# Optimization experiments

Measured on AMD Instinct MI355X. Metric: run time of the kernel, lower is better.

The kernel has to match this reference:

```python
import jax, jax.numpy as jnp
import numpy as np


def _conv1x1(x, w, b):
    # x: (B,C,H,W), w: (O,C), b: (O,)
    return jnp.einsum('bchw,oc->bohw', x, w) + b[None, :, None, None]


def setup_inputs() -> dict:
    key = jax.random.key(0)
    ks = jax.random.split(key, 10)
    B, C, H, W = 8, 64, 64, 64
    x = jax.random.normal(ks[0], (B, C, H, W), dtype=jnp.float32)
    s = 0.05
    params = {}
    names = ['wq', 'wQ', 'wK', 'wV']
    for i, n in enumerate(names):
        params[n] = jax.random.normal(ks[1 + 2 * i], (C, C), dtype=jnp.float32) * s
        params['b' + n[1:]] = jax.random.normal(ks[2 + 2 * i], (C,), dtype=jnp.float32) * s
    return dict(x=x, wq=params['wq'], bq=params['bq'], wQ=params['wQ'], bQ=params['bQ'],
                wK=params['wK'], bK=params['bK'], wV=params['wV'], bV=params['bV'],
                gamma=jnp.ones((1,), dtype=jnp.float32))


def reference(x, wq, bq, wQ, bQ, wK, bK, wV, bV, gamma):
    B, C, H, W = x.shape
    # q = query_conv(x).view(B,-1,W,H)  (pure reshape, matches torch .view on contiguous tensor)
    q = _conv1x1(x, wq, bq).reshape(B, C, W, H)
    # 2x2 average pool, stride 2
    qp = q.reshape(B, C, W // 2, 2, H // 2, 2).mean(axis=(3, 5))
    q_ = qp.reshape(B, C, (W * H) // 4)          # (B, C, N/4)
    K = _conv1x1(x, wK, bK).reshape(B, C, H * W)  # (B, C, N)
    V = _conv1x1(x, wV, bV).reshape(B, C, H * W)  # (B, C, N)
    # stage 1: pooled queries attend over all keys
    attn1 = jax.nn.softmax(jnp.einsum('bcp,bcn->bpn', q_, K), axis=-1)  # (B, N/4, N)
    out = jnp.einsum('bcn,bpn->bcp', V, attn1)                           # (B, C, N/4)
    # stage 2: full queries attend over pooled anchors
    Q = _conv1x1(x, wQ, bQ).reshape(B, C, H * W)                         # (B, C, N)
    attn2 = jax.nn.softmax(jnp.einsum('bcn,bcp->bnp', Q, q_), axis=-1)   # (B, N, N/4)
    out = jnp.einsum('bcp,bnp->bcn', out, attn2)                         # (B, C, N)
    out = out.reshape(B, C, H, W)
    return gamma * out + x
```

## Files before the change

### kernel.cpp

```cpp
#include <hip/hip_runtime.h>
#include <hip/hip_bf16.h>


typedef float  f32x4  __attribute__((ext_vector_type(4)));
typedef __bf16 bf16x8 __attribute__((ext_vector_type(8)));
typedef __bf16 bf16x4 __attribute__((ext_vector_type(4)));

__device__ __forceinline__ int swz(int ch) { return ch ^ ((ch >> 3) & 7); }

__global__ __launch_bounds__(256) void conv4_kernel(
    const float* __restrict__ x,
    const float* __restrict__ wq, const float* __restrict__ bq,
    const float* __restrict__ wQ, const float* __restrict__ bQ,
    const float* __restrict__ wK, const float* __restrict__ bK,
    const float* __restrict__ wV, const float* __restrict__ bV,
    __bf16* __restrict__ Kt, __bf16* __restrict__ Vc,
    __bf16* __restrict__ Qt, __bf16* __restrict__ qt)
{
  __shared__ float xs[64 * 132];
  __shared__ float wsh[64 * 68];

  const int tid = threadIdx.x;
  const int m   = blockIdx.x >> 8;
  const int b   = (blockIdx.x >> 5) & 7;
  const int rp  = blockIdx.x & 31;
  const int n0  = rp << 7;

  const float* wg = (m == 0) ? wK : (m == 1) ? wV : (m == 2) ? wQ : wq;
  const float* bg = (m == 0) ? bK : (m == 1) ? bV : (m == 2) ? bQ : bq;

  for (int i = tid; i < 64 * 32; i += 256) {
    int c = i >> 5, j = i & 31;
    *(f32x4*)&xs[c * 132 + j * 4] =
        *(const f32x4*)&x[((size_t)(b * 64 + c)) * 4096 + n0 + j * 4];
  }
  for (int i = tid; i < 1024; i += 256) {
    int o = i >> 4, c0 = (i & 15) << 2;
    f32x4 v = *(const f32x4*)&wg[o * 64 + c0];
    wsh[(c0 + 0) * 68 + o] = v[0];
    wsh[(c0 + 1) * 68 + o] = v[1];
    wsh[(c0 + 2) * 68 + o] = v[2];
    wsh[(c0 + 3) * 68 + o] = v[3];
  }
  __syncthreads();

  const int ty = tid >> 4, tx = tid & 15;

  float acc[4][8];
  {
    f32x4 bv = *(const f32x4*)&bg[ty * 4];
#pragma unroll
    for (int i = 0; i < 4; ++i)
#pragma unroll
      for (int j = 0; j < 8; ++j) acc[i][j] = bv[i];
  }

#pragma unroll 4
  for (int c = 0; c < 64; ++c) {
    f32x4 wv = *(const f32x4*)&wsh[c * 68 + ty * 4];
    f32x4 xa = *(const f32x4*)&xs[c * 132 + tx * 8];
    f32x4 xb = *(const f32x4*)&xs[c * 132 + tx * 8 + 4];
#pragma unroll
    for (int i = 0; i < 4; ++i) {
#pragma unroll
      for (int j = 0; j < 4; ++j) {
        acc[i][j]     += wv[i] * xa[j];
        acc[i][j + 4] += wv[i] * xb[j];
      }
    }
  }

  if (m == 0 || m == 2) {
    __bf16* dst = (m == 0) ? Kt : Qt;
#pragma unroll
    for (int j = 0; j < 8; ++j) {
      int n = n0 + tx * 8 + j;
      bf16x4 pk;
#pragma unroll
      for (int i = 0; i < 4; ++i) pk[i] = (__bf16)acc[i][j];
      *(bf16x4*)&dst[((size_t)(b * 4096 + n)) * 64 + ty * 4] = pk;
    }
  } else if (m == 1) {
#pragma unroll
    for (int i = 0; i < 4; ++i) {
      int o = ty * 4 + i;
      bf16x8 pk;
#pragma unroll
      for (int j = 0; j < 8; ++j) pk[j] = (__bf16)acc[i][j];
      *(bf16x8*)&Vc[((size_t)(b * 64 + o)) * 4096 + n0 + tx * 8] = pk;
    }
  } else {
    float pl[4][4];
#pragma unroll
    for (int i = 0; i < 4; ++i)
#pragma unroll
      for (int jj = 0; jj < 4; ++jj)
        pl[i][jj] = acc[i][2 * jj] + acc[i][2 * jj + 1];
#pragma unroll
    for (int i = 0; i < 4; ++i)
#pragma unroll
      for (int jj = 0; jj < 4; ++jj)
        pl[i][jj] += __shfl_xor(pl[i][jj], 8);
    if (tx < 8) {
#pragma unroll
      for (int jj = 0; jj < 4; ++jj) {
        int p = rp * 32 + tx * 4 + jj;
        bf16x4 pk;
#pragma unroll
        for (int i = 0; i < 4; ++i) pk[i] = (__bf16)(0.25f * pl[i][jj]);
        *(bf16x4*)&qt[((size_t)(b * 1024 + p)) * 64 + ty * 4] = pk;
      }
    }
  }
}

__global__ __launch_bounds__(512, 2) void attn1_kernel(
    const __bf16* __restrict__ Qg,
    const __bf16* __restrict__ Kg,
    const __bf16* __restrict__ Vg,
    __bf16* __restrict__ partOb,
    float* __restrict__ partL)
{
  __shared__ __align__(16) char smem[65536];

  const int tid = threadIdx.x;
  const int w = tid >> 6, lane = tid & 63;
  const int lg = (lane >> 4) & 3, lp = lane & 15;
  const int b   = blockIdx.x >> 6;
  const int qb  = (blockIdx.x >> 4) & 3;
  const int ks  = blockIdx.x & 15;

  bf16x8 qf[2][2];
#pragma unroll
  for (int qs = 0; qs < 2; ++qs) {
    const __bf16* qg =
        Qg + ((size_t)(b * 1024 + qb * 256 + w * 32 + qs * 16 + lp)) * 64;
    qf[qs][0] = *(const bf16x8*)(qg + lg * 8);
    qf[qs][1] = *(const bf16x8*)(qg + 32 + lg * 8);
  }

  f32x4 acc[2][4];
#pragma unroll
  for (int qs = 0; qs < 2; ++qs)
#pragma unroll
    for (int ct = 0; ct < 4; ++ct) acc[qs][ct] = (f32x4){0.f, 0.f, 0.f, 0.f};
  float l_run[2] = {0.f, 0.f};

  bf16x8 kreg, vreg;
  const int swt = swz(tid);
  auto load_tile = [&](int r) {
    const int kv0 = ks * 256 + r * 64;
    kreg = *(const bf16x8*)(Kg + ((size_t)(b * 4096 + kv0 + (tid >> 3))) * 64 +
                            (tid & 7) * 8);
    vreg = *(const bf16x8*)(Vg + ((size_t)(b * 64 + (tid >> 3))) * 4096 + kv0 +
                            (tid & 7) * 8);
  };
  auto write_tile = [&](int nb) {
    *(bf16x8*)((__bf16*)(smem + nb * 8192) + swt * 8) = kreg;
    *(bf16x8*)((__bf16*)(smem + 16384 + nb * 8192) + swt * 8) = vreg;
  };

  load_tile(0); write_tile(0); load_tile(1);
  __syncthreads();

  for (int r = 0; r < 4; ++r) {
    const int cur = r & 1;
    if (r + 1 < 4) write_tile(cur ^ 1);
    if (r + 2 < 4) load_tile(r + 2);

    const __bf16* lK = (const __bf16*)(smem + cur * 8192);
    const __bf16* lV = (const __bf16*)(smem + 16384 + cur * 8192);
    __bf16* lP = (__bf16*)(smem + 32768) + w * 2048;

    bf16x8 ka[4][2];
#pragma unroll
    for (int mt = 0; mt < 4; ++mt) {
      int ch0 = (mt * 16 + lp) * 8 + lg;
      ka[mt][0] = *(const bf16x8*)(lK + swz(ch0) * 8);
      ka[mt][1] = *(const bf16x8*)(lK + swz(ch0 + 4) * 8);
    }

#pragma unroll
    for (int qs = 0; qs < 2; ++qs) {
      f32x4 S[4];
#pragma unroll
      for (int mt = 0; mt < 4; ++mt) {
        f32x4 z = (f32x4){0.f, 0.f, 0.f, 0.f};
        z = __builtin_amdgcn_mfma_f32_16x16x32_bf16(ka[mt][0], qf[qs][0], z, 0, 0, 0);
        z = __builtin_amdgcn_mfma_f32_16x16x32_bf16(ka[mt][1], qf[qs][1], z, 0, 0, 0);
        S[mt] = z;
      }

      float rs = 0.f;
#pragma unroll
      for (int mt = 0; mt < 4; ++mt)
#pragma unroll
        for (int rr = 0; rr < 4; ++rr) {
          float e = __expf(S[mt][rr]);
          S[mt][rr] = e;
          rs += e;
        }
      rs += __shfl_xor(rs, 16);
      rs += __shfl_xor(rs, 32);
      l_run[qs] += rs;

#pragma unroll
      for (int mt = 0; mt < 4; ++mt) {
        bf16x4 pk;
#pragma unroll
        for (int rr = 0; rr < 4; ++rr) pk[rr] = (__bf16)S[mt][rr];
        int boff = (qs * 16 + lp) * 128 + mt * 32 + lg * 8;
        *(bf16x4*)((char*)lP + (boff ^ ((lp & 7) << 4))) = pk;
      }
    }

    bf16x8 pf[2][2];
#pragma unroll
    for (int qs = 0; qs < 2; ++qs) {
      int chp = (qs * 16 + lp) * 8 + lg;
      pf[qs][0] = *(const bf16x8*)(lP + swz(chp) * 8);
      pf[qs][1] = *(const bf16x8*)(lP + swz(chp + 4) * 8);
    }
#pragma unroll
    for (int ct = 0; ct < 4; ++ct) {
      int chv = (ct * 16 + lp) * 8 + lg;
      bf16x8 v0 = *(const bf16x8*)(lV + swz(chv) * 8);
      bf16x8 v1 = *(const bf16x8*)(lV + swz(chv + 4) * 8);
#pragma unroll
      for (int qs = 0; qs < 2; ++qs) {
        acc[qs][ct] = __builtin_amdgcn_mfma_f32_16x16x32_bf16(v0, pf[qs][0], acc[qs][ct], 0, 0, 0);
        acc[qs][ct] = __builtin_amdgcn_mfma_f32_16x16x32_bf16(v1, pf[qs][1], acc[qs][ct], 0, 0, 0);
      }
    }
    __syncthreads();
  }

  const int gq = w * 32;
  const size_t pbase = (size_t)((b * 4 + qb) * 16 + ks);
  if (lg == 0) {
#pragma unroll
    for (int qs = 0; qs < 2; ++qs)
      partL[pbase * 256 + gq + qs * 16 + lp] = l_run[qs];
  }
  __bf16* po = partOb + pbase * 16384;
#pragma unroll
  for (int qs = 0; qs < 2; ++qs)
#pragma unroll
    for (int ct = 0; ct < 4; ++ct)
#pragma unroll
      for (int rr = 0; rr < 4; ++rr)
        po[(ct * 16 + lg * 4 + rr) * 256 + gq + qs * 16 + lp] =
            (__bf16)acc[qs][ct][rr];
}

__global__ __launch_bounds__(256) void combine1_kernel(
    const __bf16* __restrict__ partOb, const float* __restrict__ partL,
    __bf16* __restrict__ O1)
{
  __shared__ float linv[256];

  const int tid = threadIdx.x;
  const int b   = blockIdx.x >> 5;
  const int qb  = (blockIdx.x >> 3) & 3;
  const int cs  = blockIdx.x & 7;
  const size_t rbase = (size_t)((b * 4 + qb) * 16);

  {
    float l = 0.f;
#pragma unroll
    for (int s = 0; s < 16; ++s) l += partL[(rbase + s) * 256 + tid];
    linv[tid] = 1.0f / l;
  }
  __syncthreads();

  const int c = cs * 8 + (tid >> 5), q8 = (tid & 31) * 8;
  float o[8] = {0.f, 0.f, 0.f, 0.f, 0.f, 0.f, 0.f, 0.f};
#pragma unroll
  for (int s = 0; s < 16; ++s) {
    bf16x8 v = *(const bf16x8*)(partOb + (rbase + s) * 16384 + c * 256 + q8);
#pragma unroll
    for (int j = 0; j < 8; ++j) o[j] += (float)v[j];
  }
  bf16x8 pk;
#pragma unroll
  for (int j = 0; j < 8; ++j) pk[j] = (__bf16)(o[j] * linv[q8 + j]);
  *(bf16x8*)(O1 + ((size_t)(b * 64 + c)) * 1024 + qb * 256 + q8) = pk;
}

__global__ __launch_bounds__(512, 2) void attn2_kernel(
    const __bf16* __restrict__ Qg,
    const __bf16* __restrict__ Kg,
    const __bf16* __restrict__ Vg,
    float* __restrict__ outp,
    const float* __restrict__ xres,
    const float* __restrict__ gammap)
{
  __shared__ __align__(16) char smem[98304];

  const int tid = threadIdx.x;
  const int w = tid >> 6, lane = tid & 63;
  const int lg = (lane >> 4) & 3, lp = lane & 15;
  const int qg4 = w & 3, ks = w >> 2;
  const int b  = blockIdx.x >> 5;
  const int q0 = (blockIdx.x & 31) * 128;

  bf16x8 qf[2][2];
#pragma unroll
  for (int qs = 0; qs < 2; ++qs) {
    const __bf16* qg =
        Qg + ((size_t)(b * 4096 + q0 + qg4 * 32 + qs * 16 + lp)) * 64;
    qf[qs][0] = *(const bf16x8*)(qg + lg * 8);
    qf[qs][1] = *(const bf16x8*)(qg + 32 + lg * 8);
  }

  f32x4 acc[2][4];
#pragma unroll
  for (int qs = 0; qs < 2; ++qs)
#pragma unroll
    for (int ct = 0; ct < 4; ++ct) acc[qs][ct] = (f32x4){0.f, 0.f, 0.f, 0.f};
  float l_run[2] = {0.f, 0.f};

  bf16x8 kreg[2], vreg[2];
  const int csi = tid & 255, sp = tid >> 8;
  const int sw0 = swz(csi), sw1 = swz(csi + 256);
  auto load_tile = [&](int r) {
    const int a0 = sp * 512 + r * 64;
#pragma unroll
    for (int j = 0; j < 2; ++j) {
      int s = csi + j * 256;
      int row = s >> 3, col = (s & 7) * 8;
      kreg[j] = *(const bf16x8*)(Kg + ((size_t)(b * 1024 + a0 + row)) * 64 + col);
      vreg[j] = *(const bf16x8*)(Vg + ((size_t)(b * 64 + row)) * 1024 + a0 + col);
    }
  };
  auto write_tile = [&](int nb) {
    __bf16* kd = (__bf16*)(smem + (sp * 2 + nb) * 8192);
    __bf16* vd = (__bf16*)(smem + 32768 + (sp * 2 + nb) * 8192);
    *(bf16x8*)(kd + sw0 * 8) = kreg[0];
    *(bf16x8*)(kd + sw1 * 8) = kreg[1];
    *(bf16x8*)(vd + sw0 * 8) = vreg[0];
    *(bf16x8*)(vd + sw1 * 8) = vreg[1];
  };

  load_tile(0); write_tile(0); load_tile(1);
  __syncthreads();

  for (int r = 0; r < 8; ++r) {
    const int cur = r & 1;
    if (r + 1 < 8) write_tile(cur ^ 1);
    if (r + 2 < 8) load_tile(r + 2);

    const __bf16* lK = (const __bf16*)(smem + (ks * 2 + cur) * 8192);
    const __bf16* lV = (const __bf16*)(smem + 32768 + (ks * 2 + cur) * 8192);
    __bf16* lP = (__bf16*)(smem + 65536) + w * 2048;

    bf16x8 ka[4][2];
#pragma unroll
    for (int mt = 0; mt < 4; ++mt) {
      int ch0 = (mt * 16 + lp) * 8 + lg;
      ka[mt][0] = *(const bf16x8*)(lK + swz(ch0) * 8);
      ka[mt][1] = *(const bf16x8*)(lK + swz(ch0 + 4) * 8);
    }

#pragma unroll
    for (int qs = 0; qs < 2; ++qs) {
      f32x4 S[4];
#pragma unroll
      for (int mt = 0; mt < 4; ++mt) {
        f32x4 z = (f32x4){0.f, 0.f, 0.f, 0.f};
        z = __builtin_amdgcn_mfma_f32_16x16x32_bf16(ka[mt][0], qf[qs][0], z, 0, 0, 0);
        z = __builtin_amdgcn_mfma_f32_16x16x32_bf16(ka[mt][1], qf[qs][1], z, 0, 0, 0);
        S[mt] = z;
      }

      float rs = 0.f;
#pragma unroll
      for (int mt = 0; mt < 4; ++mt)
#pragma unroll
        for (int rr = 0; rr < 4; ++rr) {
          float e = __expf(S[mt][rr]);
          S[mt][rr] = e;
          rs += e;
        }
      rs += __shfl_xor(rs, 16);
      rs += __shfl_xor(rs, 32);
      l_run[qs] += rs;

#pragma unroll
      for (int mt = 0; mt < 4; ++mt) {
        bf16x4 pk;
#pragma unroll
        for (int rr = 0; rr < 4; ++rr) pk[rr] = (__bf16)S[mt][rr];
        int boff = (qs * 16 + lp) * 128 + mt * 32 + lg * 8;
        *(bf16x4*)((char*)lP + (boff ^ ((lp & 7) << 4))) = pk;
      }
    }

    bf16x8 pf[2][2];
#pragma unroll
    for (int qs = 0; qs < 2; ++qs) {
      int chp = (qs * 16 + lp) * 8 + lg;
      pf[qs][0] = *(const bf16x8*)(lP + swz(chp) * 8);
      pf[qs][1] = *(const bf16x8*)(lP + swz(chp + 4) * 8);
    }
#pragma unroll
    for (int ct = 0; ct < 4; ++ct) {
      int chv = (ct * 16 + lp) * 8 + lg;
      bf16x8 v0 = *(const bf16x8*)(lV + swz(chv) * 8);
      bf16x8 v1 = *(const bf16x8*)(lV + swz(chv + 4) * 8);
#pragma unroll
      for (int qs = 0; qs < 2; ++qs) {
        acc[qs][ct] = __builtin_amdgcn_mfma_f32_16x16x32_bf16(v0, pf[qs][0], acc[qs][ct], 0, 0, 0);
        acc[qs][ct] = __builtin_amdgcn_mfma_f32_16x16x32_bf16(v1, pf[qs][1], acc[qs][ct], 0, 0, 0);
      }
    }
    __syncthreads();
  }

  float* cb = (float*)smem;
  float* lb = (float*)(smem + 69632);
  if (lg == 0) {
#pragma unroll
    for (int qs = 0; qs < 2; ++qs)
      lb[w * 32 + qs * 16 + lp] = l_run[qs];
  }
  {
    float* myc = cb + w * 2176;
#pragma unroll
    for (int qs = 0; qs < 2; ++qs)
#pragma unroll
      for (int ct = 0; ct < 4; ++ct)
        *(f32x4*)(myc + (qs * 16 + lp) * 68 + ct * 16 + lg * 4) = acc[qs][ct];
  }
  __syncthreads();

  if (w < 4) {
    const int g = w;
    const float g0 = gammap[0];
#pragma unroll
    for (int qs = 0; qs < 2; ++qs) {
      const int qq = qs * 16 + lp;
      const int nq = q0 + g * 32 + qq;
      float inv = 1.0f / (lb[g * 32 + qq] + lb[(g + 4) * 32 + qq]);
#pragma unroll
      for (int ct = 0; ct < 4; ++ct) {
        f32x4 t0 = *(const f32x4*)(cb + g * 2176 + qq * 68 + ct * 16 + lg * 4);
        f32x4 t1 = *(const f32x4*)(cb + (g + 4) * 2176 + qq * 68 + ct * 16 + lg * 4);
        f32x4 o = t0 + t1;
#pragma unroll
        for (int rr = 0; rr < 4; ++rr) {
          int c = ct * 16 + lg * 4 + rr;
          size_t oi = ((size_t)(b * 64 + c)) * 4096 + nq;
          outp[oi] = g0 * (o[rr] * inv) + xres[oi];
        }
      }
    }
  }
}

extern "C" void kernel_launch(void* const* d_in, const int* in_sizes, int n_in,
                              void* d_out, int out_size, void* d_ws, size_t ws_size,
                              hipStream_t stream) {
  const float* x     = (const float*)d_in[0];
  const float* wq    = (const float*)d_in[1];
  const float* bq    = (const float*)d_in[2];
  const float* wQ    = (const float*)d_in[3];
  const float* bQ    = (const float*)d_in[4];
  const float* wK    = (const float*)d_in[5];
  const float* bK    = (const float*)d_in[6];
  const float* wV    = (const float*)d_in[7];
  const float* bV    = (const float*)d_in[8];
  const float* gamma = (const float*)d_in[9];

  __bf16* ws = (__bf16*)d_ws;
  __bf16* Kt = ws;
  __bf16* Vc = ws + 2097152;
  __bf16* Qt = ws + 4194304;
  __bf16* qt = ws + 6291456;
  __bf16* O1 = ws + 6815744;
  __bf16* partOb1 = (__bf16*)((char*)d_ws + (16ull << 20));
  float*  partL1  = (float*)((char*)d_ws + (33ull << 20));

  hipLaunchKernelGGL(conv4_kernel, dim3(1024), dim3(256), 0, stream,
                     x, wq, bq, wQ, bQ, wK, bK, wV, bV, Kt, Vc, Qt, qt);
  hipLaunchKernelGGL(attn1_kernel, dim3(512), dim3(512), 0, stream,
                     qt, Kt, Vc, partOb1, partL1);
  hipLaunchKernelGGL(combine1_kernel, dim3(256), dim3(256), 0, stream,
                     partOb1, partL1, O1);
  hipLaunchKernelGGL(attn2_kernel, dim3(256), dim3(512), 0, stream,
                     Qt, qt, O1, (float*)d_out, x, gamma);
}
```

Baseline: 66.52 us.

## Read V fragments directly from global memory and transpose PV MFMA output layout

In both attention kernels, V tiles are no longer staged through shared memory. Each wave loads its V MFMA fragments straight from global memory, relying on V's channel-major layout, and swaps the MFMA operand order so the accumulator comes out transposed. That layout lets the partial-output stores and the final residual epilogue use vectorized bf16x4/f32x4 accesses, and it shrinks LDS usage. The cost is redundant global/L2 reads of V across waves, issued on the critical path without prefetching.

```diff
diff --git a/kernel.cpp b/kernel.cpp
--- a/kernel.cpp
+++ b/kernel.cpp
@@ -121,7 +121,7 @@
     __bf16* __restrict__ partOb,
     float* __restrict__ partL)
 {
-  __shared__ __align__(16) char smem[65536];
+  __shared__ __align__(16) char smem[49152];
 
   const int tid = threadIdx.x;
   const int w = tid >> 6, lane = tid & 63;
@@ -146,18 +146,15 @@
     for (int ct = 0; ct < 4; ++ct) acc[qs][ct] = (f32x4){0.f, 0.f, 0.f, 0.f};
   float l_run[2] = {0.f, 0.f};
 
-  bf16x8 kreg, vreg;
+  bf16x8 kreg;
   const int swt = swz(tid);
   auto load_tile = [&](int r) {
     const int kv0 = ks * 256 + r * 64;
     kreg = *(const bf16x8*)(Kg + ((size_t)(b * 4096 + kv0 + (tid >> 3))) * 64 +
                             (tid & 7) * 8);
-    vreg = *(const bf16x8*)(Vg + ((size_t)(b * 64 + (tid >> 3))) * 4096 + kv0 +
-                            (tid & 7) * 8);
   };
   auto write_tile = [&](int nb) {
     *(bf16x8*)((__bf16*)(smem + nb * 8192) + swt * 8) = kreg;
-    *(bf16x8*)((__bf16*)(smem + 16384 + nb * 8192) + swt * 8) = vreg;
   };
 
   load_tile(0); write_tile(0); load_tile(1);
@@ -168,9 +165,9 @@
     if (r + 1 < 4) write_tile(cur ^ 1);
     if (r + 2 < 4) load_tile(r + 2);
 
+    const int kv0 = ks * 256 + r * 64;
     const __bf16* lK = (const __bf16*)(smem + cur * 8192);
-    const __bf16* lV = (const __bf16*)(smem + 16384 + cur * 8192);
-    __bf16* lP = (__bf16*)(smem + 32768) + w * 2048;
+    __bf16* lP = (__bf16*)(smem + 16384) + w * 2048;
 
     bf16x8 ka[4][2];
 #pragma unroll
@@ -223,13 +220,13 @@
     }
 #pragma unroll
     for (int ct = 0; ct < 4; ++ct) {
-      int chv = (ct * 16 + lp) * 8 + lg;
-      bf16x8 v0 = *(const bf16x8*)(lV + swz(chv) * 8);
-      bf16x8 v1 = *(const bf16x8*)(lV + swz(chv + 4) * 8);
+      const __bf16* vr = Vg + ((size_t)(b * 64 + ct * 16 + lp)) * 4096 + kv0 + lg * 8;
+      bf16x8 vf0 = *(const bf16x8*)(vr);
+      bf16x8 vf1 = *(const bf16x8*)(vr + 32);
 #pragma unroll
       for (int qs = 0; qs < 2; ++qs) {
-        acc[qs][ct] = __builtin_amdgcn_mfma_f32_16x16x32_bf16(v0, pf[qs][0], acc[qs][ct], 0, 0, 0);
-        acc[qs][ct] = __builtin_amdgcn_mfma_f32_16x16x32_bf16(v1, pf[qs][1], acc[qs][ct], 0, 0, 0);
+        acc[qs][ct] = __builtin_amdgcn_mfma_f32_16x16x32_bf16(pf[qs][0], vf0, acc[qs][ct], 0, 0, 0);
+        acc[qs][ct] = __builtin_amdgcn_mfma_f32_16x16x32_bf16(pf[qs][1], vf1, acc[qs][ct], 0, 0, 0);
       }
     }
     __syncthreads();
@@ -246,11 +243,12 @@
 #pragma unroll
   for (int qs = 0; qs < 2; ++qs)
 #pragma unroll
-    for (int ct = 0; ct < 4; ++ct)
-#pragma unroll
-      for (int rr = 0; rr < 4; ++rr)
-        po[(ct * 16 + lg * 4 + rr) * 256 + gq + qs * 16 + lp] =
-            (__bf16)acc[qs][ct][rr];
+    for (int ct = 0; ct < 4; ++ct) {
+      bf16x4 pk;
+#pragma unroll
+      for (int rr = 0; rr < 4; ++rr) pk[rr] = (__bf16)acc[qs][ct][rr];
+      *(bf16x4*)&po[(ct * 16 + lp) * 256 + gq + qs * 16 + lg * 4] = pk;
+    }
 }
 
 __global__ __launch_bounds__(256) void combine1_kernel(
@@ -295,7 +293,7 @@
     const float* __restrict__ xres,
     const float* __restrict__ gammap)
 {
-  __shared__ __align__(16) char smem[98304];
+  __shared__ __align__(16) char smem[74752];
 
   const int tid = threadIdx.x;
   const int w = tid >> 6, lane = tid & 63;
@@ -320,7 +318,7 @@
     for (int ct = 0; ct < 4; ++ct) acc[qs][ct] = (f32x4){0.f, 0.f, 0.f, 0.f};
   float l_run[2] = {0.f, 0.f};
 
-  bf16x8 kreg[2], vreg[2];
+  bf16x8 kreg[2];
   const int csi = tid & 255, sp = tid >> 8;
   const int sw0 = swz(csi), sw1 = swz(csi + 256);
   auto load_tile = [&](int r) {
@@ -330,16 +328,12 @@
       int s = csi + j * 256;
       int row = s >> 3, col = (s & 7) * 8;
       kreg[j] = *(const bf16x8*)(Kg + ((size_t)(b * 1024 + a0 + row)) * 64 + col);
-      vreg[j] = *(const bf16x8*)(Vg + ((size_t)(b * 64 + row)) * 1024 + a0 + col);
     }
   };
   auto write_tile = [&](int nb) {
     __bf16* kd = (__bf16*)(smem + (sp * 2 + nb) * 8192);
-    __bf16* vd = (__bf16*)(smem + 32768 + (sp * 2 + nb) * 8192);
     *(bf16x8*)(kd + sw0 * 8) = kreg[0];
     *(bf16x8*)(kd + sw1 * 8) = kreg[1];
-    *(bf16x8*)(vd + sw0 * 8) = vreg[0];
-    *(bf16x8*)(vd + sw1 * 8) = vreg[1];
   };
 
   load_tile(0); write_tile(0); load_tile(1);
@@ -350,9 +344,9 @@
     if (r + 1 < 8) write_tile(cur ^ 1);
     if (r + 2 < 8) load_tile(r + 2);
 
+    const int kv0 = ks * 512 + r * 64;
     const __bf16* lK = (const __bf16*)(smem + (ks * 2 + cur) * 8192);
-    const __bf16* lV = (const __bf16*)(smem + 32768 + (ks * 2 + cur) * 8192);
-    __bf16* lP = (__bf16*)(smem + 65536) + w * 2048;
+    __bf16* lP = (__bf16*)(smem + 32768) + w * 2048;
 
     bf16x8 ka[4][2];
 #pragma unroll
@@ -405,32 +399,32 @@
     }
 #pragma unroll
     for (int ct = 0; ct < 4; ++ct) {
-      int chv = (ct * 16 + lp) * 8 + lg;
-      bf16x8 v0 = *(const bf16x8*)(lV + swz(chv) * 8);
-      bf16x8 v1 = *(const bf16x8*)(lV + swz(chv + 4) * 8);
+      const __bf16* vr = Vg + ((size_t)(b * 64 + ct * 16 + lp)) * 1024 + kv0 + lg * 8;
+      bf16x8 vf0 = *(const bf16x8*)(vr);
+      bf16x8 vf1 = *(const bf16x8*)(vr + 32);
 #pragma unroll
       for (int qs = 0; qs < 2; ++qs) {
-        acc[qs][ct] = __builtin_amdgcn_mfma_f32_16x16x32_bf16(v0, pf[qs][0], acc[qs][ct], 0, 0, 0);
-        acc[qs][ct] = __builtin_amdgcn_mfma_f32_16x16x32_bf16(v1, pf[qs][1], acc[qs][ct], 0, 0, 0);
+        acc[qs][ct] = __builtin_amdgcn_mfma_f32_16x16x32_bf16(pf[qs][0], vf0, acc[qs][ct], 0, 0, 0);
+        acc[qs][ct] = __builtin_amdgcn_mfma_f32_16x16x32_bf16(pf[qs][1], vf1, acc[qs][ct], 0, 0, 0);
       }
     }
     __syncthreads();
   }
 
   float* cb = (float*)smem;
-  float* lb = (float*)(smem + 69632);
+  float* lb = (float*)(smem + 73728);
   if (lg == 0) {
 #pragma unroll
     for (int qs = 0; qs < 2; ++qs)
       lb[w * 32 + qs * 16 + lp] = l_run[qs];
   }
   {
-    float* myc = cb + w * 2176;
+    float* myc = cb + w * 2304;
 #pragma unroll
     for (int qs = 0; qs < 2; ++qs)
 #pragma unroll
       for (int ct = 0; ct < 4; ++ct)
-        *(f32x4*)(myc + (qs * 16 + lp) * 68 + ct * 16 + lg * 4) = acc[qs][ct];
+        *(f32x4*)(myc + (ct * 16 + lp) * 36 + qs * 16 + lg * 4) = acc[qs][ct];
   }
   __syncthreads();
 
@@ -439,20 +433,24 @@
     const float g0 = gammap[0];
 #pragma unroll
     for (int qs = 0; qs < 2; ++qs) {
-      const int qq = qs * 16 + lp;
-      const int nq = q0 + g * 32 + qq;
-      float inv = 1.0f / (lb[g * 32 + qq] + lb[(g + 4) * 32 + qq]);
+      f32x4 lv0 = *(const f32x4*)(lb + g * 32 + qs * 16 + lg * 4);
+      f32x4 lv1 = *(const f32x4*)(lb + (g + 4) * 32 + qs * 16 + lg * 4);
+      f32x4 inv4;
+#pragma unroll
+      for (int j = 0; j < 4; ++j) inv4[j] = 1.0f / (lv0[j] + lv1[j]);
 #pragma unroll
       for (int ct = 0; ct < 4; ++ct) {
-        f32x4 t0 = *(const f32x4*)(cb + g * 2176 + qq * 68 + ct * 16 + lg * 4);
-        f32x4 t1 = *(const f32x4*)(cb + (g + 4) * 2176 + qq * 68 + ct * 16 + lg * 4);
-        f32x4 o = t0 + t1;
-#pragma unroll
-        for (int rr = 0; rr < 4; ++rr) {
-          int c = ct * 16 + lg * 4 + rr;
-          size_t oi = ((size_t)(b * 64 + c)) * 4096 + nq;
-          outp[oi] = g0 * (o[rr] * inv) + xres[oi];
-        }
+        int coff = (ct * 16 + lp) * 36 + qs * 16 + lg * 4;
+        f32x4 t0 = *(const f32x4*)(cb + g * 2304 + coff);
+        f32x4 t1 = *(const f32x4*)(cb + (g + 4) * 2304 + coff);
+        size_t oi = ((size_t)(b * 64 + ct * 16 + lp)) * 4096 + q0 + g * 32 +
+                    qs * 16 + lg * 4;
+        f32x4 xr = *(const f32x4*)(xres + oi);
+        f32x4 res;
+#pragma unroll
+        for (int j = 0; j < 4; ++j)
+          res[j] = g0 * ((t0[j] + t1[j]) * inv4[j]) + xr[j];
+        *(f32x4*)(outp + oi) = res;
       }
     }
   }
```

Result: slower. 81.88 us (+23.1%).
